# Kernel tuning notes

Measured on AMD Instinct MI355X. Metric: run time of the kernel, lower is better.

## Reference

```python
import jax, jax.numpy as jnp
import numpy as np

N_NODES = 50000
N_EDGES = 800000
ENT_DIM = 128
REL_DIM = 128
NUM_REL = 200  # relation table has 2*NUM_REL rows (forward + inverse)


def setup_inputs() -> dict:
    key = jax.random.key(0)
    ks = jax.random.split(key, 16)
    inp = {
        'src': jax.random.randint(ks[0], (N_EDGES,), 0, N_NODES),
        'dst': jax.random.randint(ks[1], (N_EDGES,), 0, N_NODES),
        'etypes': jax.random.randint(ks[2], (N_EDGES,), 0, 2 * NUM_REL),
        'ent_emb': jax.random.normal(ks[3], (N_NODES, ENT_DIM), jnp.float32),
        'rel_emb': jax.random.normal(ks[4], (2 * NUM_REL, REL_DIM), jnp.float32),
        'W_O_w': jax.random.normal(ks[5], (ENT_DIM, REL_DIM + ENT_DIM), jnp.float32) * 0.05,
        'W_O_b': jax.random.normal(ks[6], (ENT_DIM,), jnp.float32) * 0.05,
        'W_I_w': jax.random.normal(ks[7], (ENT_DIM, REL_DIM + ENT_DIM), jnp.float32) * 0.05,
        'W_I_b': jax.random.normal(ks[8], (ENT_DIM,), jnp.float32) * 0.05,
        'W_S_w': jax.random.normal(ks[9], (ENT_DIM, ENT_DIM), jnp.float32) * 0.05,
        'W_S_b': jax.random.normal(ks[10], (ENT_DIM,), jnp.float32) * 0.05,
        'W_R_w': jax.random.normal(ks[11], (REL_DIM, REL_DIM), jnp.float32) * 0.05,
        'W_R_b': jax.random.normal(ks[12], (REL_DIM,), jnp.float32) * 0.05,
    }
    return inp


def reference(src, dst, etypes, ent_emb, rel_emb,
              W_O_w, W_O_b, W_I_w, W_I_b, W_S_w, W_S_b, W_R_w, W_R_b):
    # msg_func: per-edge gather of relation emb and source node emb, concat,
    # then route through W_O (type < num_rel) or W_I (type >= num_rel).
    comp_h = jnp.concatenate([rel_emb[etypes], ent_emb[src]], axis=-1)  # [E, rel+ent]
    msg_o = comp_h @ W_O_w.T + W_O_b  # [E, ent]
    msg_i = comp_h @ W_I_w.T + W_I_b
    non_inv = (etypes < NUM_REL)[:, None]
    msg = jnp.where(non_inv, msg_o, msg_i)
    # fn.mean('msg','h_agg'): scatter-mean into destination nodes (0 if no in-edges)
    agg_sum = jax.ops.segment_sum(msg, dst, num_segments=N_NODES)
    deg = jax.ops.segment_sum(jnp.ones((msg.shape[0],), msg.dtype), dst,
                              num_segments=N_NODES)
    h_agg = agg_sum / jnp.maximum(deg, 1.0)[:, None]
    # apply_node_func (act is None -> identity)
    ent_new = ent_emb @ W_S_w.T + W_S_b + h_agg
    # edge_update
    rel_new = rel_emb @ W_R_w.T + W_R_b
    return ent_new, rel_new
```

## Files before the change

kernel.cpp:

```cpp
#include <hip/hip_runtime.h>
#include <hip/hip_bf16.h>

#define N_NODES 50000
#define N_EDGES 800000
#define DIM 128
#define NUM_REL 200
#define NREL2 (2 * NUM_REL)
#define NROWG (N_NODES / 16)
#define NBLK_G ((NROWG + 7) / 8)
#define FILL_NB 1024
#define NCHUNK5 ((N_EDGES + 511) / 512)
#define NODES_PER_XCD (N_NODES / 8)
#define CAP 64
#define ZROW (2 * N_NODES)
#define ZREL NREL2
#define ZPAY (ZROW | (ZREL << 17))

typedef __bf16 bf16x8 __attribute__((ext_vector_type(8)));
typedef float f32x4 __attribute__((ext_vector_type(4)));

__global__ void __launch_bounds__(256)
prep_rel_kernel(const float* __restrict__ rel_emb,
                const float* __restrict__ W_O_w, const float* __restrict__ W_O_b,
                const float* __restrict__ W_I_w, const float* __restrict__ W_I_b,
                const float* __restrict__ W_R_w, const float* __restrict__ W_R_b,
                const float* __restrict__ W_S_w,
                __bf16* __restrict__ WTh, __bf16* __restrict__ WTl,
                int* __restrict__ counts, __bf16* __restrict__ EEb,
                __bf16* __restrict__ Rb, float* __restrict__ rel_new) {
    const int bid = blockIdx.x;
    if (bid < NREL2 / 2) {
        __shared__ float row[2][DIM];
        const int h = threadIdx.x >> 7;
        const int j = threadIdx.x & 127;
        const int t = bid * 2 + h;
        row[h][j] = rel_emb[t * DIM + j];
        __syncthreads();

        const bool fwd = (t < NUM_REL);
        const float* __restrict__ wSel = (fwd ? W_O_w : W_I_w) + j * (2 * DIM);
        const float* __restrict__ wR = W_R_w + j * DIM;
        float aSel = 0.f, aR = 0.f;
#pragma unroll 8
        for (int k = 0; k < DIM; ++k) {
            const float e = row[h][k];
            aSel += e * wSel[k];
            aR += e * wR[k];
        }
        Rb[t * DIM + j] = (__bf16)(aSel + (fwd ? W_O_b[j] : W_I_b[j]));
        rel_new[t * DIM + j] = aR + W_R_b[j];
    } else {
        const int idx = (bid - NREL2 / 2) * 256 + threadIdx.x;
        if (idx < 384 * DIM) {
            const int j = idx >> 7;
            const int k = idx & 127;
            float v;
            if (j < 128) v = W_O_w[j * (2 * DIM) + DIM + k];
            else if (j < 256) v = W_I_w[(j - 128) * (2 * DIM) + DIM + k];
            else v = W_S_w[(j - 256) * DIM + k];
            const __bf16 h = (__bf16)v;
            WTh[idx] = h;
            WTl[idx] = (__bf16)(v - (float)h);
        }
        if (idx < N_NODES) counts[idx] = 0;
        if (idx < DIM) {
            EEb[(size_t)ZROW * DIM + idx] = (__bf16)0.f;
            Rb[(size_t)ZREL * DIM + idx] = (__bf16)0.f;
        }
    }
}

#define REP4(F) F(0) F(1) F(2) F(3)

__global__ void __launch_bounds__(512, 1)
gemm_fill_kernel(const float* __restrict__ ent,
                 const __bf16* __restrict__ WTh, const __bf16* __restrict__ WTl,
                 const float* __restrict__ W_S_b,
                 __bf16* __restrict__ EEb, float* __restrict__ ent_S,
                 const int* __restrict__ src, const int* __restrict__ dst,
                 const int* __restrict__ et, int* __restrict__ counts,
                 int* __restrict__ sp) {
    __shared__ __bf16 LBh[16 * 64 * 8];
    __shared__ __bf16 LBl[16 * 64 * 8];

    if (blockIdx.x >= NBLK_G) {
        const int fb = blockIdx.x - NBLK_G;
        const int r = blockIdx.x & 7;
#pragma unroll 1
        for (int c = fb >> 3; c < NCHUNK5; c += FILL_NB / 8) {
            const int e = c * 512 + threadIdx.x;
            if (e < N_EDGES) {
                const int d = dst[e];
                if ((unsigned)(d - r * NODES_PER_XCD) < (unsigned)NODES_PER_XCD) {
                    const int t = et[e];
                    const int row = src[e] + ((t < NUM_REL) ? 0 : N_NODES);
                    const int pos = atomicAdd(&counts[d], 1);
                    if (pos < CAP) sp[(d << 6) + pos] = row | (t << 17);
                }
            }
        }
        return;
    }

    const int tid = threadIdx.x;
    const int wv = tid >> 6;
    const int rg = blockIdx.x * 8 + wv;
    const bool valid = (rg < NROWG);
    const int rgc = valid ? rg : (NROWG - 1);
    const int l = tid & 63;
    const int r16 = l & 15;
    const int kg = l >> 4;

    const float* __restrict__ aptr = ent + (size_t)(rgc * 16 + r16) * DIM + kg * 8;
#define ADECL(ks)                                                              \
    bf16x8 ah##ks, al##ks;                                                     \
    {                                                                          \
        const float4 v0 = *(const float4*)(aptr + (ks) * 32);                  \
        const float4 v1 = *(const float4*)(aptr + (ks) * 32 + 4);              \
        const float xs[8] = {v0.x, v0.y, v0.z, v0.w, v1.x, v1.y, v1.z, v1.w};  \
        _Pragma("unroll") for (int i = 0; i < 8; ++i) {                        \
            const __bf16 h = (__bf16)xs[i];                                    \
            ah##ks[i] = h;                                                     \
            al##ks[i] = (__bf16)(xs[i] - (float)h);                            \
        }                                                                      \
    }
    REP4(ADECL)
#undef ADECL

    const int orow = rgc * 16 + kg * 4;

#pragma unroll 1
    for (int cb = 0; cb < 6; ++cb) {
        __syncthreads();
#pragma unroll
        for (int i = 0; i < 2; ++i) {
            const int g = i * 512 + tid;
            const int sks = g >> 6;
            const int ls = g & 63;
            const int s = sks >> 2;
            const int ks = sks & 3;
            const size_t soff =
                (size_t)(cb * 64 + s * 16 + (ls & 15)) * DIM + ks * 32 + (ls >> 4) * 8;
            *(bf16x8*)(&LBh[g * 8]) = *(const bf16x8*)(WTh + soff);
            *(bf16x8*)(&LBl[g * 8]) = *(const bf16x8*)(WTl + soff);
        }
        __syncthreads();

        f32x4 p0 = {0.f, 0.f, 0.f, 0.f}, q0 = {0.f, 0.f, 0.f, 0.f};
        f32x4 p1 = {0.f, 0.f, 0.f, 0.f}, q1 = {0.f, 0.f, 0.f, 0.f};
        f32x4 p2 = {0.f, 0.f, 0.f, 0.f}, q2 = {0.f, 0.f, 0.f, 0.f};
        f32x4 p3 = {0.f, 0.f, 0.f, 0.f}, q3 = {0.f, 0.f, 0.f, 0.f};

#define KS(ks)                                                                 \
    {                                                                          \
        const bf16x8 bh0 = *(const bf16x8*)(&LBh[((0 * 4 + (ks)) * 64 + l) * 8]); \
        const bf16x8 bh1 = *(const bf16x8*)(&LBh[((1 * 4 + (ks)) * 64 + l) * 8]); \
        const bf16x8 bh2 = *(const bf16x8*)(&LBh[((2 * 4 + (ks)) * 64 + l) * 8]); \
        const bf16x8 bh3 = *(const bf16x8*)(&LBh[((3 * 4 + (ks)) * 64 + l) * 8]); \
        const bf16x8 bl0 = *(const bf16x8*)(&LBl[((0 * 4 + (ks)) * 64 + l) * 8]); \
        const bf16x8 bl1 = *(const bf16x8*)(&LBl[((1 * 4 + (ks)) * 64 + l) * 8]); \
        const bf16x8 bl2 = *(const bf16x8*)(&LBl[((2 * 4 + (ks)) * 64 + l) * 8]); \
        const bf16x8 bl3 = *(const bf16x8*)(&LBl[((3 * 4 + (ks)) * 64 + l) * 8]); \
        p0 = __builtin_amdgcn_mfma_f32_16x16x32_bf16(ah##ks, bh0, p0, 0, 0, 0); \
        p1 = __builtin_amdgcn_mfma_f32_16x16x32_bf16(ah##ks, bh1, p1, 0, 0, 0); \
        p2 = __builtin_amdgcn_mfma_f32_16x16x32_bf16(ah##ks, bh2, p2, 0, 0, 0); \
        p3 = __builtin_amdgcn_mfma_f32_16x16x32_bf16(ah##ks, bh3, p3, 0, 0, 0); \
        q0 = __builtin_amdgcn_mfma_f32_16x16x32_bf16(al##ks, bh0, q0, 0, 0, 0); \
        q1 = __builtin_amdgcn_mfma_f32_16x16x32_bf16(al##ks, bh1, q1, 0, 0, 0); \
        q2 = __builtin_amdgcn_mfma_f32_16x16x32_bf16(al##ks, bh2, q2, 0, 0, 0); \
        q3 = __builtin_amdgcn_mfma_f32_16x16x32_bf16(al##ks, bh3, q3, 0, 0, 0); \
        q0 = __builtin_amdgcn_mfma_f32_16x16x32_bf16(ah##ks, bl0, q0, 0, 0, 0); \
        q1 = __builtin_amdgcn_mfma_f32_16x16x32_bf16(ah##ks, bl1, q1, 0, 0, 0); \
        q2 = __builtin_amdgcn_mfma_f32_16x16x32_bf16(ah##ks, bl2, q2, 0, 0, 0); \
        q3 = __builtin_amdgcn_mfma_f32_16x16x32_bf16(ah##ks, bl3, q3, 0, 0, 0); \
    }
        REP4(KS)
#undef KS

        if (valid) {
            const int colb = (cb & 1) * 64;
            if (cb < 4) {
                __bf16* __restrict__ obb =
                    EEb + ((cb < 2) ? 0 : (size_t)N_NODES * DIM);
#define ST(s, P, Q)                                                            \
                {                                                              \
                    const int col = colb + (s) * 16 + r16;                     \
                    const f32x4 a = P + Q;                                     \
                    obb[(size_t)(orow + 0) * DIM + col] = (__bf16)a[0];        \
                    obb[(size_t)(orow + 1) * DIM + col] = (__bf16)a[1];        \
                    obb[(size_t)(orow + 2) * DIM + col] = (__bf16)a[2];        \
                    obb[(size_t)(orow + 3) * DIM + col] = (__bf16)a[3];        \
                }
                ST(0, p0, q0) ST(1, p1, q1) ST(2, p2, q2) ST(3, p3, q3)
#undef ST
            } else {
#define ST(s, P, Q)                                                            \
                {                                                              \
                    const int col = colb + (s) * 16 + r16;                     \
                    const float bs = W_S_b[col];                               \
                    const f32x4 a = P + Q;                                     \
                    ent_S[(size_t)(orow + 0) * DIM + col] = a[0] + bs;         \
                    ent_S[(size_t)(orow + 1) * DIM + col] = a[1] + bs;         \
                    ent_S[(size_t)(orow + 2) * DIM + col] = a[2] + bs;         \
                    ent_S[(size_t)(orow + 3) * DIM + col] = a[3] + bs;         \
                }
                ST(0, p0, q0) ST(1, p1, q1) ST(2, p2, q2) ST(3, p3, q3)
#undef ST
            }
        }
    }
}

__global__ void __launch_bounds__(256)
gather_kernel(const int* __restrict__ counts, const int* __restrict__ sp,
              const __bf16* __restrict__ EEb, const __bf16* __restrict__ Rb,
              const float* __restrict__ ent_S, float* __restrict__ out_ent) {
    const int node = blockIdx.x * 4 + (threadIdx.x >> 6);
    if (node >= N_NODES) return;
    const int l = threadIdx.x & 63;
    const int q = l >> 4;
    const int m = l & 15;

    const int cntT = counts[node];
    const int cnt = min(cntT, CAP);

    float a0 = 0.f, a1 = 0.f, a2 = 0.f, a3 = 0.f;
    float a4 = 0.f, a5 = 0.f, a6 = 0.f, a7 = 0.f;
    const char* __restrict__ Eb = (const char*)EEb + 16 * m;
    const char* __restrict__ Rp = (const char*)Rb + 16 * m;

    const int myp = (l < cnt) ? sp[(node << 6) + l] : ZPAY;
#pragma unroll 2
    for (int i = 0; i < cnt; i += 4) {
        const int p = __shfl(myp, i + q);
        const unsigned eoff = (unsigned)(p & 0x1FFFF) << 8;
        const unsigned roff = ((unsigned)p >> 17) << 8;
        const uint4 ev = *(const uint4*)(Eb + eoff);
        const uint4 rv = *(const uint4*)(Rp + roff);
        a0 += __uint_as_float(ev.x << 16) + __uint_as_float(rv.x << 16);
        a1 += __uint_as_float(ev.x & 0xffff0000u) +
              __uint_as_float(rv.x & 0xffff0000u);
        a2 += __uint_as_float(ev.y << 16) + __uint_as_float(rv.y << 16);
        a3 += __uint_as_float(ev.y & 0xffff0000u) +
              __uint_as_float(rv.y & 0xffff0000u);
        a4 += __uint_as_float(ev.z << 16) + __uint_as_float(rv.z << 16);
        a5 += __uint_as_float(ev.z & 0xffff0000u) +
              __uint_as_float(rv.z & 0xffff0000u);
        a6 += __uint_as_float(ev.w << 16) + __uint_as_float(rv.w << 16);
        a7 += __uint_as_float(ev.w & 0xffff0000u) +
              __uint_as_float(rv.w & 0xffff0000u);
    }

#define RED(A) A += __shfl_xor(A, 16); A += __shfl_xor(A, 32);
    RED(a0) RED(a1) RED(a2) RED(a3) RED(a4) RED(a5) RED(a6) RED(a7)
#undef RED

    if (l < 16) {
        const float inv = 1.0f / fmaxf((float)cntT, 1.0f);
        const float* sp_ = ent_S + (size_t)node * DIM + 8 * m;
        const float4 s0 = *(const float4*)(sp_);
        const float4 s1 = *(const float4*)(sp_ + 4);
        float4 o0, o1;
        o0.x = s0.x + a0 * inv;
        o0.y = s0.y + a1 * inv;
        o0.z = s0.z + a2 * inv;
        o0.w = s0.w + a3 * inv;
        o1.x = s1.x + a4 * inv;
        o1.y = s1.y + a5 * inv;
        o1.z = s1.z + a6 * inv;
        o1.w = s1.w + a7 * inv;
        float* op = out_ent + (size_t)node * DIM + 8 * m;
        *(float4*)(op) = o0;
        *(float4*)(op + 4) = o1;
    }
}

extern "C" void kernel_launch(void* const* d_in, const int* in_sizes, int n_in,
                              void* d_out, int out_size, void* d_ws, size_t ws_size,
                              hipStream_t stream) {
    const int* src = (const int*)d_in[0];
    const int* dst = (const int*)d_in[1];
    const int* et = (const int*)d_in[2];
    const float* ent_emb = (const float*)d_in[3];
    const float* rel_emb = (const float*)d_in[4];
    const float* W_O_w = (const float*)d_in[5];
    const float* W_O_b = (const float*)d_in[6];
    const float* W_I_w = (const float*)d_in[7];
    const float* W_I_b = (const float*)d_in[8];
    const float* W_S_w = (const float*)d_in[9];
    const float* W_S_b = (const float*)d_in[10];
    const float* W_R_w = (const float*)d_in[11];
    const float* W_R_b = (const float*)d_in[12];

    float* out_ent = (float*)d_out;
    float* out_rel = out_ent + (size_t)N_NODES * DIM;

    float* wsf = (float*)d_ws;
    float* ent_S = wsf;
    wsf += (size_t)N_NODES * DIM;
    __bf16* EEb = (__bf16*)wsf;
    wsf += ((size_t)(2 * N_NODES + 1) * DIM + 1) / 2;
    __bf16* Rb = (__bf16*)wsf;
    wsf += (size_t)(NREL2 + 1) * DIM / 2;
    __bf16* WTh = (__bf16*)wsf;
    wsf += 384 * DIM / 2;
    __bf16* WTl = (__bf16*)wsf;
    wsf += 384 * DIM / 2;
    int* counts = (int*)wsf;
    int* sp = counts + N_NODES;

    prep_rel_kernel<<<NREL2 / 2 + 196, 256, 0, stream>>>(
        rel_emb, W_O_w, W_O_b, W_I_w, W_I_b, W_R_w, W_R_b, W_S_w,
        WTh, WTl, counts, EEb, Rb, out_rel);

    gemm_fill_kernel<<<NBLK_G + FILL_NB, 512, 0, stream>>>(
        ent_emb, WTh, WTl, W_S_b, EEb, ent_S, src, dst, et, counts, sp);

    gather_kernel<<<(N_NODES + 3) / 4, 256, 0, stream>>>(counts, sp, EEb, Rb,
                                                         ent_S, out_ent);
}
```

Before: 111.1 us.

## Use atomic work-stealing pool for edge fill shared by GEMM and fill blocks

Replaces the static strided assignment of edge chunks to dedicated fill blocks with a per-XCD atomic chunk counter (pool) that every block, including GEMM blocks after they finish, claims work from. The number of dedicated fill blocks drops from 1024 to 633, and the pool counters are zeroed in the prep kernel. This is meant to balance the GEMM and bucketing phases dynamically so that no block sits idle. In exchange each 512-edge chunk now costs an extra global atomic plus two block barriers, and every block keeps scanning until its XCD's counter runs out.

```diff
diff --git a/kernel.cpp b/kernel.cpp
--- a/kernel.cpp
+++ b/kernel.cpp
@@ -8,7 +8,7 @@
 #define NREL2 (2 * NUM_REL)
 #define NROWG (N_NODES / 16)
 #define NBLK_G ((NROWG + 7) / 8)
-#define FILL_NB 1024
+#define FILL_NB 633
 #define NCHUNK5 ((N_EDGES + 511) / 512)
 #define NODES_PER_XCD (N_NODES / 8)
 #define CAP 64
@@ -26,8 +26,9 @@
                 const float* __restrict__ W_R_w, const float* __restrict__ W_R_b,
                 const float* __restrict__ W_S_w,
                 __bf16* __restrict__ WTh, __bf16* __restrict__ WTl,
-                int* __restrict__ counts, __bf16* __restrict__ EEb,
-                __bf16* __restrict__ Rb, float* __restrict__ rel_new) {
+                int* __restrict__ counts, int* __restrict__ pool,
+                __bf16* __restrict__ EEb, __bf16* __restrict__ Rb,
+                float* __restrict__ rel_new) {
     const int bid = blockIdx.x;
     if (bid < NREL2 / 2) {
         __shared__ float row[2][DIM];
@@ -63,6 +64,7 @@
             WTl[idx] = (__bf16)(v - (float)h);
         }
         if (idx < N_NODES) counts[idx] = 0;
+        if (idx < 8) pool[idx] = 0;
         if (idx < DIM) {
             EEb[(size_t)ZROW * DIM + idx] = (__bf16)0.f;
             Rb[(size_t)ZREL * DIM + idx] = (__bf16)0.f;
@@ -79,77 +81,61 @@
                  __bf16* __restrict__ EEb, float* __restrict__ ent_S,
                  const int* __restrict__ src, const int* __restrict__ dst,
                  const int* __restrict__ et, int* __restrict__ counts,
-                 int* __restrict__ sp) {
+                 int* __restrict__ sp, int* __restrict__ pool) {
     __shared__ __bf16 LBh[16 * 64 * 8];
     __shared__ __bf16 LBl[16 * 64 * 8];
-
-    if (blockIdx.x >= NBLK_G) {
-        const int fb = blockIdx.x - NBLK_G;
-        const int r = blockIdx.x & 7;
+    __shared__ int claim;
+
+    if (blockIdx.x < NBLK_G) {
+        const int tid = threadIdx.x;
+        const int wv = tid >> 6;
+        const int rg = blockIdx.x * 8 + wv;
+        const bool valid = (rg < NROWG);
+        const int rgc = valid ? rg : (NROWG - 1);
+        const int l = tid & 63;
+        const int r16 = l & 15;
+        const int kg = l >> 4;
+
+        const float* __restrict__ aptr =
+            ent + (size_t)(rgc * 16 + r16) * DIM + kg * 8;
+#define ADECL(ks)                                                              \
+        bf16x8 ah##ks, al##ks;                                                 \
+        {                                                                      \
+            const float4 v0 = *(const float4*)(aptr + (ks) * 32);              \
+            const float4 v1 = *(const float4*)(aptr + (ks) * 32 + 4);          \
+            const float xs[8] = {v0.x, v0.y, v0.z, v0.w, v1.x, v1.y, v1.z, v1.w}; \
+            _Pragma("unroll") for (int i = 0; i < 8; ++i) {                    \
+                const __bf16 h = (__bf16)xs[i];                                \
+                ah##ks[i] = h;                                                 \
+                al##ks[i] = (__bf16)(xs[i] - (float)h);                        \
+            }                                                                  \
+        }
+        REP4(ADECL)
+#undef ADECL
+
+        const int orow = rgc * 16 + kg * 4;
+
 #pragma unroll 1
-        for (int c = fb >> 3; c < NCHUNK5; c += FILL_NB / 8) {
-            const int e = c * 512 + threadIdx.x;
-            if (e < N_EDGES) {
-                const int d = dst[e];
-                if ((unsigned)(d - r * NODES_PER_XCD) < (unsigned)NODES_PER_XCD) {
-                    const int t = et[e];
-                    const int row = src[e] + ((t < NUM_REL) ? 0 : N_NODES);
-                    const int pos = atomicAdd(&counts[d], 1);
-                    if (pos < CAP) sp[(d << 6) + pos] = row | (t << 17);
-                }
+        for (int cb = 0; cb < 6; ++cb) {
+            __syncthreads();
+#pragma unroll
+            for (int i = 0; i < 2; ++i) {
+                const int g = i * 512 + tid;
+                const int sks = g >> 6;
+                const int ls = g & 63;
+                const int s = sks >> 2;
+                const int ks = sks & 3;
+                const size_t soff = (size_t)(cb * 64 + s * 16 + (ls & 15)) * DIM
+                                    + ks * 32 + (ls >> 4) * 8;
+                *(bf16x8*)(&LBh[g * 8]) = *(const bf16x8*)(WTh + soff);
+                *(bf16x8*)(&LBl[g * 8]) = *(const bf16x8*)(WTl + soff);
             }
-        }
-        return;
-    }
-
-    const int tid = threadIdx.x;
-    const int wv = tid >> 6;
-    const int rg = blockIdx.x * 8 + wv;
-    const bool valid = (rg < NROWG);
-    const int rgc = valid ? rg : (NROWG - 1);
-    const int l = tid & 63;
-    const int r16 = l & 15;
-    const int kg = l >> 4;
-
-    const float* __restrict__ aptr = ent + (size_t)(rgc * 16 + r16) * DIM + kg * 8;
-#define ADECL(ks)                                                              \
-    bf16x8 ah##ks, al##ks;                                                     \
-    {                                                                          \
-        const float4 v0 = *(const float4*)(aptr + (ks) * 32);                  \
-        const float4 v1 = *(const float4*)(aptr + (ks) * 32 + 4);              \
-        const float xs[8] = {v0.x, v0.y, v0.z, v0.w, v1.x, v1.y, v1.z, v1.w};  \
-        _Pragma("unroll") for (int i = 0; i < 8; ++i) {                        \
-            const __bf16 h = (__bf16)xs[i];                                    \
-            ah##ks[i] = h;                                                     \
-            al##ks[i] = (__bf16)(xs[i] - (float)h);                            \
-        }                                                                      \
-    }
-    REP4(ADECL)
-#undef ADECL
-
-    const int orow = rgc * 16 + kg * 4;
-
-#pragma unroll 1
-    for (int cb = 0; cb < 6; ++cb) {
-        __syncthreads();
-#pragma unroll
-        for (int i = 0; i < 2; ++i) {
-            const int g = i * 512 + tid;
-            const int sks = g >> 6;
-            const int ls = g & 63;
-            const int s = sks >> 2;
-            const int ks = sks & 3;
-            const size_t soff =
-                (size_t)(cb * 64 + s * 16 + (ls & 15)) * DIM + ks * 32 + (ls >> 4) * 8;
-            *(bf16x8*)(&LBh[g * 8]) = *(const bf16x8*)(WTh + soff);
-            *(bf16x8*)(&LBl[g * 8]) = *(const bf16x8*)(WTl + soff);
-        }
-        __syncthreads();
-
-        f32x4 p0 = {0.f, 0.f, 0.f, 0.f}, q0 = {0.f, 0.f, 0.f, 0.f};
-        f32x4 p1 = {0.f, 0.f, 0.f, 0.f}, q1 = {0.f, 0.f, 0.f, 0.f};
-        f32x4 p2 = {0.f, 0.f, 0.f, 0.f}, q2 = {0.f, 0.f, 0.f, 0.f};
-        f32x4 p3 = {0.f, 0.f, 0.f, 0.f}, q3 = {0.f, 0.f, 0.f, 0.f};
+            __syncthreads();
+
+            f32x4 p0 = {0.f, 0.f, 0.f, 0.f}, q0 = {0.f, 0.f, 0.f, 0.f};
+            f32x4 p1 = {0.f, 0.f, 0.f, 0.f}, q1 = {0.f, 0.f, 0.f, 0.f};
+            f32x4 p2 = {0.f, 0.f, 0.f, 0.f}, q2 = {0.f, 0.f, 0.f, 0.f};
+            f32x4 p3 = {0.f, 0.f, 0.f, 0.f}, q3 = {0.f, 0.f, 0.f, 0.f};
 
 #define KS(ks)                                                                 \
     {                                                                          \
@@ -174,38 +160,59 @@
         q2 = __builtin_amdgcn_mfma_f32_16x16x32_bf16(ah##ks, bl2, q2, 0, 0, 0); \
         q3 = __builtin_amdgcn_mfma_f32_16x16x32_bf16(ah##ks, bl3, q3, 0, 0, 0); \
     }
-        REP4(KS)
+            REP4(KS)
 #undef KS
 
-        if (valid) {
-            const int colb = (cb & 1) * 64;
-            if (cb < 4) {
-                __bf16* __restrict__ obb =
-                    EEb + ((cb < 2) ? 0 : (size_t)N_NODES * DIM);
+            if (valid) {
+                const int colb = (cb & 1) * 64;
+                if (cb < 4) {
+                    __bf16* __restrict__ obb =
+                        EEb + ((cb < 2) ? 0 : (size_t)N_NODES * DIM);
 #define ST(s, P, Q)                                                            \
-                {                                                              \
-                    const int col = colb + (s) * 16 + r16;                     \
-                    const f32x4 a = P + Q;                                     \
-                    obb[(size_t)(orow + 0) * DIM + col] = (__bf16)a[0];        \
-                    obb[(size_t)(orow + 1) * DIM + col] = (__bf16)a[1];        \
-                    obb[(size_t)(orow + 2) * DIM + col] = (__bf16)a[2];        \
-                    obb[(size_t)(orow + 3) * DIM + col] = (__bf16)a[3];        \
+                    {                                                          \
+                        const int col = colb + (s) * 16 + r16;                 \
+                        const f32x4 a = P + Q;                                 \
+                        obb[(size_t)(orow + 0) * DIM + col] = (__bf16)a[0];    \
+                        obb[(size_t)(orow + 1) * DIM + col] = (__bf16)a[1];    \
+                        obb[(size_t)(orow + 2) * DIM + col] = (__bf16)a[2];    \
+                        obb[(size_t)(orow + 3) * DIM + col] = (__bf16)a[3];    \
+                    }
+                    ST(0, p0, q0) ST(1, p1, q1) ST(2, p2, q2) ST(3, p3, q3)
+#undef ST
+                } else {
+#define ST(s, P, Q)                                                            \
+                    {                                                          \
+                        const int col = colb + (s) * 16 + r16;                 \
+                        const float bs = W_S_b[col];                           \
+                        const f32x4 a = P + Q;                                 \
+                        ent_S[(size_t)(orow + 0) * DIM + col] = a[0] + bs;     \
+                        ent_S[(size_t)(orow + 1) * DIM + col] = a[1] + bs;     \
+                        ent_S[(size_t)(orow + 2) * DIM + col] = a[2] + bs;     \
+                        ent_S[(size_t)(orow + 3) * DIM + col] = a[3] + bs;     \
+                    }
+                    ST(0, p0, q0) ST(1, p1, q1) ST(2, p2, q2) ST(3, p3, q3)
+#undef ST
                 }
-                ST(0, p0, q0) ST(1, p1, q1) ST(2, p2, q2) ST(3, p3, q3)
-#undef ST
-            } else {
-#define ST(s, P, Q)                                                            \
-                {                                                              \
-                    const int col = colb + (s) * 16 + r16;                     \
-                    const float bs = W_S_b[col];                               \
-                    const f32x4 a = P + Q;                                     \
-                    ent_S[(size_t)(orow + 0) * DIM + col] = a[0] + bs;         \
-                    ent_S[(size_t)(orow + 1) * DIM + col] = a[1] + bs;         \
-                    ent_S[(size_t)(orow + 2) * DIM + col] = a[2] + bs;         \
-                    ent_S[(size_t)(orow + 3) * DIM + col] = a[3] + bs;         \
-                }
-                ST(0, p0, q0) ST(1, p1, q1) ST(2, p2, q2) ST(3, p3, q3)
-#undef ST
+            }
+        }
+    }
+
+    const int r = blockIdx.x & 7;
+    const int rlo = r * NODES_PER_XCD;
+    for (;;) {
+        __syncthreads();
+        if (threadIdx.x == 0) claim = atomicAdd(&pool[r], 1);
+        __syncthreads();
+        const int c = claim;
+        if (c >= NCHUNK5) break;
+        const int e = c * 512 + threadIdx.x;
+        if (e < N_EDGES) {
+            const int d = dst[e];
+            if ((unsigned)(d - rlo) < (unsigned)NODES_PER_XCD) {
+                const int t = et[e];
+                const int row = src[e] + ((t < NUM_REL) ? 0 : N_NODES);
+                const int pos = atomicAdd(&counts[d], 1);
+                if (pos < CAP) sp[(d << 6) + pos] = row | (t << 17);
             }
         }
     }
@@ -307,14 +314,15 @@
     __bf16* WTl = (__bf16*)wsf;
     wsf += 384 * DIM / 2;
     int* counts = (int*)wsf;
-    int* sp = counts + N_NODES;
+    int* pool = counts + N_NODES;
+    int* sp = pool + 8;
 
     prep_rel_kernel<<<NREL2 / 2 + 196, 256, 0, stream>>>(
         rel_emb, W_O_w, W_O_b, W_I_w, W_I_b, W_R_w, W_R_b, W_S_w,
-        WTh, WTl, counts, EEb, Rb, out_rel);
+        WTh, WTl, counts, pool, EEb, Rb, out_rel);
 
     gemm_fill_kernel<<<NBLK_G + FILL_NB, 512, 0, stream>>>(
-        ent_emb, WTh, WTl, W_S_b, EEb, ent_S, src, dst, et, counts, sp);
+        ent_emb, WTh, WTl, W_S_b, EEb, ent_S, src, dst, et, counts, sp, pool);
 
     gather_kernel<<<(N_NODES + 3) / 4, 256, 0, stream>>>(counts, sp, EEb, Rb,
                                                          ent_S, out_ent);
```

After: 223.9 us. 101% more time.
